# Performance work log

Measured on AMD Instinct MI355X. Metric: run time of the kernel, lower is better.

## Reference

```python
import jax, jax.numpy as jnp
import numpy as np

B, T = 256, 800
D_IN, H, L, V = 128, 512, 2, 128


def setup_inputs() -> dict:
    key = jax.random.key(0)
    ks = jax.random.split(key, 12)
    s = 0.1  # init scale for stability
    return {
        "W_ih0": jax.random.normal(ks[0], (4 * H, D_IN), jnp.float32) * s,
        "W_hh0": jax.random.normal(ks[1], (4 * H, H), jnp.float32) * s,
        "b_ih0": jax.random.normal(ks[2], (4 * H,), jnp.float32) * s,
        "b_hh0": jax.random.normal(ks[3], (4 * H,), jnp.float32) * s,
        "W_ih1": jax.random.normal(ks[4], (4 * H, H), jnp.float32) * s,
        "W_hh1": jax.random.normal(ks[5], (4 * H, H), jnp.float32) * s,
        "b_ih1": jax.random.normal(ks[6], (4 * H,), jnp.float32) * s,
        "b_hh1": jax.random.normal(ks[7], (4 * H,), jnp.float32) * s,
        "W_lin": jax.random.normal(ks[8], (V, H), jnp.float32) * s,
        "b_lin": jax.random.normal(ks[9], (V,), jnp.float32) * s,
        "z": jax.random.randint(ks[10], (B, T), 0, V, jnp.int32),
        "num_frames": jax.random.randint(ks[11], (B,), 100, 800, jnp.int32),
    }


def _lstm_log_prob(layers, W_lin, b_lin, z, num_frames):
    # teacher-forced inputs: step i sees one_hot(z[:, i-1]), zeros at i=0
    oh = jax.nn.one_hot(z[:, :-1], D_IN, dtype=jnp.float32)          # [B, T-1, D]
    inputs = jnp.concatenate([jnp.zeros((B, 1, D_IN), jnp.float32), oh], axis=1)
    inputs = jnp.transpose(inputs, (1, 0, 2))                         # [T, B, D]

    def step(carry, x_t):
        h, c = carry  # each [L, B, H]
        inp = x_t
        hs, cs = [], []
        for l, (Wih, Whh, bih, bhh) in enumerate(layers):
            gates = inp @ Wih.T + h[l] @ Whh.T + bih + bhh            # [B, 4H]
            i, f, g, o = jnp.split(gates, 4, axis=-1)                 # torch gate order i,f,g,o
            c_new = jax.nn.sigmoid(f) * c[l] + jax.nn.sigmoid(i) * jnp.tanh(g)
            h_new = jax.nn.sigmoid(o) * jnp.tanh(c_new)
            hs.append(h_new)
            cs.append(c_new)
            inp = h_new
        logits_t = inp @ W_lin.T + b_lin                              # [B, V]
        return (jnp.stack(hs), jnp.stack(cs)), logits_t

    h0 = jnp.zeros((L, B, H), jnp.float32)
    c0 = jnp.zeros((L, B, H), jnp.float32)
    _, logits = jax.lax.scan(step, (h0, c0), inputs)                  # [T, B, V]
    logits = jnp.transpose(logits, (1, 0, 2))                         # [B, T, V]

    logp = jax.nn.log_softmax(logits, axis=-1)
    nll = -jnp.take_along_axis(logp, z[..., None].astype(jnp.int32), axis=-1)[..., 0]  # [B, T]
    mask = (jnp.arange(T)[None, :] < num_frames[:, None]).astype(nll.dtype)
    return (nll * mask).mean(axis=-1)                                 # [B] (mean over full T, as in torch)


def reference(W_ih0, W_hh0, b_ih0, b_hh0, W_ih1, W_hh1, b_ih1, b_hh1, W_lin, b_lin, z, num_frames):
    layers = [(W_ih0, W_hh0, b_ih0, b_hh0), (W_ih1, W_hh1, b_ih1, b_hh1)]
    return _lstm_log_prob(layers, W_lin, b_lin, z, num_frames)
```

## Files before the change

kernel.cpp:

```cpp
#include <hip/hip_runtime.h>

#define TT 800

typedef __attribute__((ext_vector_type(8))) short bf16x8;
typedef __attribute__((ext_vector_type(4))) float f32x4;
typedef unsigned short u16;
typedef unsigned int u32;
typedef unsigned long long u64;

constexpr int NCW = 128, NWG = 136, RT = 32;
constexpr size_t WL0A_OFF = 0;
constexpr size_t WL0B_OFF = 2097152;
constexpr size_t WL1_OFF  = 2621440;
constexpr size_t WLIN_OFF = 6815744;
constexpr size_t H0_OFF   = 6946816;
constexpr size_t H1_OFF   = 7471104;
constexpr size_t BAR_OFF  = 7995392;
constexpr int HB = 256 * 512;
constexpr int A_ST = 520;
constexpr int G_OFF_B = 33280;
constexpr int P_OFF_B = 49792;
constexpr int LDS_BYTES = 53248;

__device__ __forceinline__ u16 f2b(float x) {
  u32 u = __float_as_uint(x);
  return (u16)((u + 0x7FFFu + ((u >> 16) & 1u)) >> 16);
}
__device__ __forceinline__ float b2f(u16 v) { return __uint_as_float(((u32)v) << 16); }
__device__ __forceinline__ float sigf(float x) { return 1.f / (1.f + __expf(-x)); }
__device__ __forceinline__ float tanh_f(float x) { float e = __expf(2.f * x); return 1.f - 2.f / (e + 1.f); }

__device__ __forceinline__ u64 ld_coh8(const u64* p) {
  return __hip_atomic_load(p, __ATOMIC_RELAXED, __HIP_MEMORY_SCOPE_AGENT);
}
__device__ __forceinline__ void st_coh8(u64* p, u64 v) {
  __hip_atomic_store(p, v, __ATOMIC_RELAXED, __HIP_MEMORY_SCOPE_AGENT);
}
__device__ __forceinline__ void fadd(u32* f) {
  __hip_atomic_fetch_add(f, 1u, __ATOMIC_RELAXED, __HIP_MEMORY_SCOPE_AGENT);
}
__device__ __forceinline__ void fpoll(u32* f, u32 thr) {
  while (__hip_atomic_load(f, __ATOMIC_RELAXED, __HIP_MEMORY_SCOPE_AGENT) < thr)
    __builtin_amdgcn_s_sleep(1);
}
__device__ __forceinline__ void fadd_l(u32* f) {
  __hip_atomic_fetch_add(f, 1u, __ATOMIC_RELAXED, __HIP_MEMORY_SCOPE_WORKGROUP);
}
__device__ __forceinline__ void fpoll_l(u32* f, u32 thr) {
  while (*(volatile u32*)f < thr) {
    __builtin_amdgcn_s_sleep(1);
    asm volatile("buffer_inv" ::: "memory");
  }
}
__device__ __forceinline__ void l1inv() { asm volatile("buffer_inv" ::: "memory"); }

__global__ void prep_kernel(const float* __restrict__ wih0, const float* __restrict__ whh0,
                            const float* __restrict__ wih1, const float* __restrict__ whh1,
                            const float* __restrict__ wlinf,
                            u16* __restrict__ wl0a, u16* __restrict__ wl0b,
                            u16* __restrict__ wl1, u16* __restrict__ wlin) {
  int i = blockIdx.x * 256 + threadIdx.x;
  const int NA = 2048 * 512, NB = 128 * 2048, N1 = 2048 * 1024, N2 = 128 * 512;
  if (i < NA) {
    int col = i >> 9, k = i & 511;
    wl0a[i] = f2b(whh0[col * 512 + k]);
  } else if (i < NA + NB) {
    int j = i - NA, k = j >> 11, col = j & 2047;
    wl0b[j] = f2b(wih0[col * 128 + k]);
  } else if (i < NA + NB + N1) {
    int j = i - NA - NB, col = j >> 10, k = j & 1023;
    float v = (k < 512) ? wih1[col * 512 + k] : whh1[col * 512 + (k - 512)];
    wl1[j] = f2b(v);
  } else if (i < NA + NB + N1 + N2) {
    int j = i - NA - NB - N1, col = j >> 9, k = j & 511;
    wlin[j] = f2b(wlinf[col * 512 + k]);
  }
}

__global__ __launch_bounds__(256, 1) void lstm_kernel(
    const float* __restrict__ bih0, const float* __restrict__ bhh0,
    const float* __restrict__ bih1, const float* __restrict__ bhh1,
    const float* __restrict__ blin,
    const int* __restrict__ z, const int* __restrict__ nfr,
    const u16* __restrict__ wl0a, const u16* __restrict__ wl0b,
    const u16* __restrict__ wl1, const u16* __restrict__ wlin,
    u16* __restrict__ h0buf, u16* __restrict__ h1buf,
    u32* __restrict__ bars, float* __restrict__ out) {
  extern __shared__ char smem[];
  u16* A = (u16*)smem;
  float* Gf = (float*)(smem + G_OFF_B);
  float* Pm = (float*)(smem + P_OFF_B);
  float* Ps = Pm + 256;
  float* Pt = Ps + 256;
  const int wg = blockIdx.x;
  const int w_all = wg >> 3;
  const bool isC = (w_all < 16);
  const int tile = wg & 7;
  const int w = isC ? w_all : 16;
  const int tid = threadIdx.x, lane = tid & 63, wv = tid >> 6;
  const int l15 = lane & 15, l4 = lane >> 4;
  const int row0 = tile * RT;
  u32* F = bars + tile * 32;
  const f32x4 VZ = {0.f, 0.f, 0.f, 0.f};
  const int rC = tid >> 3, u0C = (tid & 7) * 4;
  const int cuL = tid & 31, rgL = tid >> 5;

  float c0s[4] = {0, 0, 0, 0}, c1s[4] = {0, 0, 0, 0};
  float accN = 0.f, nflv = 0.f;
  float bias0c[2], bias1c[2], biasLc[2];
  bf16x8 bq0R[32];
  bf16x8 bq1R[64];
  bf16x8 wlR[32];

  if (isC) {
#pragma unroll
    for (int cb = 0; cb < 2; ++cb) {
      int col = wv * 512 + w * 32 + cb * 16 + l15;
      bias0c[cb] = bih0[col] + bhh0[col];
      bias1c[cb] = bih1[col] + bhh1[col];
      const u16* b0 = wl0a + (size_t)col * 512 + l4 * 8;
#pragma unroll
      for (int kb = 0; kb < 16; ++kb) bq0R[cb * 16 + kb] = *(const bf16x8*)(b0 + kb * 32);
      const u16* b1 = wl1 + (size_t)col * 1024 + l4 * 8;
#pragma unroll
      for (int kb = 0; kb < 32; ++kb) bq1R[cb * 32 + kb] = *(const bf16x8*)(b1 + kb * 32);
    }
  } else {
#pragma unroll
    for (int cb = 0; cb < 2; ++cb) {
      int colV = wv * 32 + cb * 16 + l15;
      biasLc[cb] = blin[colV];
      const u16* bL = wlin + (size_t)colV * 512 + l4 * 8;
#pragma unroll
      for (int kb = 0; kb < 16; ++kb) wlR[cb * 16 + kb] = *(const bf16x8*)(bL + kb * 32);
    }
    if (rgL == 0) nflv = (float)nfr[row0 + cuL];
  }

  u32 xcc;
  asm volatile("s_getreg_b32 %0, hwreg(HW_REG_XCC_ID)" : "=s"(xcc));
  {
    int* hls = (int*)Pm;
    if (tid == 0) {
      u32 bit = 1u << (xcc & 31u);
      __hip_atomic_fetch_or(bars + 256 + tile, bit, __ATOMIC_RELAXED, __HIP_MEMORY_SCOPE_AGENT);
      __hip_atomic_fetch_add(bars + 272, 1u, __ATOMIC_RELAXED, __HIP_MEMORY_SCOPE_AGENT);
      while (__hip_atomic_load(bars + 272, __ATOMIC_RELAXED, __HIP_MEMORY_SCOPE_AGENT) < (u32)NWG)
        __builtin_amdgcn_s_sleep(1);
      u32 m = __hip_atomic_load(bars + 256 + tile, __ATOMIC_RELAXED, __HIP_MEMORY_SCOPE_AGENT);
      hls[0] = (m == bit) ? 1 : 0;
    }
    __syncthreads();
    const_cast<volatile int&>(hls[0]);
  }
  const bool lok = (((volatile int*)Pm)[0] != 0);
  __syncthreads();

  if (isC && w == 0) {
    u64* z0 = (u64*)(h0buf + HB + row0 * 512);
    u64* z1 = (u64*)(h1buf + row0 * 512);
    u64* z2 = (u64*)(h1buf + HB + row0 * 512);
    if (lok) {
      for (int k = tid; k < 2048; k += 256) { z0[k] = 0; z1[k] = 0; z2[k] = 0; }
    } else {
      for (int k = tid; k < 2048; k += 256) { st_coh8(z0 + k, 0); st_coh8(z1 + k, 0); st_coh8(z2 + k, 0); }
    }
  }
  __syncthreads();
  if (tid == 0) { if (lok) fadd_l(F); else fadd(F); }

  auto ldA = [&](int rb, int kb) {
    return *(const bf16x8*)(A + (rb * 16 + l15) * A_ST + kb * 32 + l4 * 8);
  };

#pragma unroll 1
  for (int tau = 0; tau <= TT + 1; ++tau) {
    if (tid == 0) { if (lok) fpoll_l(F, 17u * (u32)(tau + 1)); else fpoll(F, 17u * (u32)(tau + 1)); }
    __syncthreads();
    if (lok) l1inv();
    const u16* h0src = h0buf + ((tau + 1) & 1) * HB + row0 * 512;
    const u64* h1s64 = (const u64*)(h1buf + (tau & 1) * HB + row0 * 512);
    const bool l0act = isC && (tau < TT);
    const bool l1act = isC && (tau >= 1 && tau <= TT);

    if (isC) {
      if (tau <= TT) {
        u64 ta[8], tb[8];
        const u64* s64 = (const u64*)h0src;
        if (lok) {
#pragma unroll
          for (int c = 0; c < 8; ++c) {
            int li = c * 256 + tid;
            ta[c] = s64[li * 2]; tb[c] = s64[li * 2 + 1];
          }
        } else {
#pragma unroll
          for (int c = 0; c < 8; ++c) {
            int li = c * 256 + tid;
            ta[c] = ld_coh8(s64 + li * 2); tb[c] = ld_coh8(s64 + li * 2 + 1);
          }
        }
#pragma unroll
        for (int c = 0; c < 8; ++c) {
          int li = c * 256 + tid, row = li >> 6, cc = li & 63;
          u64* d = (u64*)(A + row * A_ST + cc * 8);
          d[0] = ta[c]; d[1] = tb[c];
        }
      }
      u64 ha[4], hb[4];
      if (l1act) {
        if (lok) {
#pragma unroll
          for (int c = 0; c < 4; ++c) {
            int li = c * 256 + tid;
            ha[c] = h1s64[li * 2]; hb[c] = h1s64[li * 2 + 1];
          }
        } else {
#pragma unroll
          for (int c = 0; c < 4; ++c) {
            int li = c * 256 + tid;
            ha[c] = ld_coh8(h1s64 + li * 2); hb[c] = ld_coh8(h1s64 + li * 2 + 1);
          }
        }
      }
      __syncthreads();

      f32x4 acc0[2][2] = {{VZ, VZ}, {VZ, VZ}};
      f32x4 acc1[2][2] = {{VZ, VZ}, {VZ, VZ}};
      if (l0act) {
#pragma unroll
        for (int kb = 0; kb < 16; ++kb) {
          bf16x8 a0 = ldA(0, kb), a1 = ldA(1, kb);
#pragma unroll
          for (int cb = 0; cb < 2; ++cb) {
            acc0[0][cb] = __builtin_amdgcn_mfma_f32_16x16x32_bf16(a0, bq0R[cb * 16 + kb], acc0[0][cb], 0, 0, 0);
            acc0[1][cb] = __builtin_amdgcn_mfma_f32_16x16x32_bf16(a1, bq0R[cb * 16 + kb], acc0[1][cb], 0, 0, 0);
          }
        }
      }
      if (l1act) {
#pragma unroll
        for (int kb = 0; kb < 16; ++kb) {
          bf16x8 a0 = ldA(0, kb), a1 = ldA(1, kb);
#pragma unroll
          for (int cb = 0; cb < 2; ++cb) {
            acc1[0][cb] = __builtin_amdgcn_mfma_f32_16x16x32_bf16(a0, bq1R[cb * 32 + kb], acc1[0][cb], 0, 0, 0);
            acc1[1][cb] = __builtin_amdgcn_mfma_f32_16x16x32_bf16(a1, bq1R[cb * 32 + kb], acc1[1][cb], 0, 0, 0);
          }
        }
      }
      if (l0act) {
#pragma unroll
        for (int rb = 0; rb < 2; ++rb)
#pragma unroll
          for (int cb = 0; cb < 2; ++cb)
#pragma unroll
            for (int q = 0; q < 4; ++q)
              Gf[(rb * 16 + l4 * 4 + q) * 129 + wv * 32 + cb * 16 + l15] = acc0[rb][cb][q] + bias0c[cb];
      }
      __syncthreads();

      u64 ha2[4], hb2[4];
      if (l1act) {
        if (lok) {
#pragma unroll
          for (int c = 0; c < 4; ++c) {
            int li = (c + 4) * 256 + tid;
            ha2[c] = h1s64[li * 2]; hb2[c] = h1s64[li * 2 + 1];
          }
        } else {
#pragma unroll
          for (int c = 0; c < 4; ++c) {
            int li = (c + 4) * 256 + tid;
            ha2[c] = ld_coh8(h1s64 + li * 2); hb2[c] = ld_coh8(h1s64 + li * 2 + 1);
          }
        }
      }
      if (l0act) {
        float g4[4][4];
#pragma unroll
        for (int g = 0; g < 4; ++g)
#pragma unroll
          for (int j = 0; j < 4; ++j) g4[g][j] = Gf[rC * 129 + g * 32 + u0C + j];
        if (tau >= 1) {
          int zr = z[(row0 + rC) * TT + (tau - 1)];
          const u16* gb = wl0b + (size_t)zr * 2048 + w * 32 + u0C;
#pragma unroll
          for (int g = 0; g < 4; ++g) {
            u64 v = *(const u64*)(gb + g * 512);
#pragma unroll
            for (int j = 0; j < 4; ++j) g4[g][j] += b2f((u16)(v >> (16 * j)));
          }
        }
        u64 pk = 0;
#pragma unroll
        for (int j = 0; j < 4; ++j) {
          float cn = sigf(g4[1][j]) * c0s[j] + sigf(g4[0][j]) * tanh_f(g4[2][j]);
          float hn = sigf(g4[3][j]) * tanh_f(cn);
          c0s[j] = cn;
          pk |= ((u64)f2b(hn)) << (16 * j);
        }
        u16* h0w = h0buf + (tau & 1) * HB + row0 * 512;
        u64* dst = (u64*)(h0w + rC * 512 + w * 32 + u0C);
        if (lok) *dst = pk; else st_coh8(dst, pk);
      }
      if (l1act) {
#pragma unroll
        for (int c = 0; c < 4; ++c) {
          int li = c * 256 + tid, row = li >> 6, cc = li & 63;
          u64* d = (u64*)(A + row * A_ST + cc * 8);
          d[0] = ha[c]; d[1] = hb[c];
        }
#pragma unroll
        for (int c = 0; c < 4; ++c) {
          int li = (c + 4) * 256 + tid, row = li >> 6, cc = li & 63;
          u64* d = (u64*)(A + row * A_ST + cc * 8);
          d[0] = ha2[c]; d[1] = hb2[c];
        }
      }
      __syncthreads();

      if (l1act) {
#pragma unroll
        for (int kb = 16; kb < 32; ++kb) {
          bf16x8 a0 = ldA(0, kb - 16), a1 = ldA(1, kb - 16);
#pragma unroll
          for (int cb = 0; cb < 2; ++cb) {
            acc1[0][cb] = __builtin_amdgcn_mfma_f32_16x16x32_bf16(a0, bq1R[cb * 32 + kb], acc1[0][cb], 0, 0, 0);
            acc1[1][cb] = __builtin_amdgcn_mfma_f32_16x16x32_bf16(a1, bq1R[cb * 32 + kb], acc1[1][cb], 0, 0, 0);
          }
        }
#pragma unroll
        for (int rb = 0; rb < 2; ++rb)
#pragma unroll
          for (int cb = 0; cb < 2; ++cb)
#pragma unroll
            for (int q = 0; q < 4; ++q)
              Gf[(rb * 16 + l4 * 4 + q) * 129 + wv * 32 + cb * 16 + l15] = acc1[rb][cb][q] + bias1c[cb];
      }
      __syncthreads();

      if (l1act) {
        float g4[4][4];
#pragma unroll
        for (int g = 0; g < 4; ++g)
#pragma unroll
          for (int j = 0; j < 4; ++j) g4[g][j] = Gf[rC * 129 + g * 32 + u0C + j];
        u64 pk = 0;
#pragma unroll
        for (int j = 0; j < 4; ++j) {
          float cn = sigf(g4[1][j]) * c1s[j] + sigf(g4[0][j]) * tanh_f(g4[2][j]);
          float hn = sigf(g4[3][j]) * tanh_f(cn);
          c1s[j] = cn;
          pk |= ((u64)f2b(hn)) << (16 * j);
        }
        u16* h1w = h1buf + ((tau + 1) & 1) * HB + row0 * 512;
        u64* dst = (u64*)(h1w + rC * 512 + w * 32 + u0C);
        if (lok) *dst = pk; else st_coh8(dst, pk);
      }
      __syncthreads();
      if (tid == 0) { if (lok) fadd_l(F); else fadd(F); }
    } else {
      const bool lgact = (tau >= 2);
      if (lgact) {
        u64 ta[8], tb[8];
        if (lok) {
#pragma unroll
          for (int c = 0; c < 8; ++c) {
            int li = c * 256 + tid;
            ta[c] = h1s64[li * 2]; tb[c] = h1s64[li * 2 + 1];
          }
        } else {
#pragma unroll
          for (int c = 0; c < 8; ++c) {
            int li = c * 256 + tid;
            ta[c] = ld_coh8(h1s64 + li * 2); tb[c] = ld_coh8(h1s64 + li * 2 + 1);
          }
        }
#pragma unroll
        for (int c = 0; c < 8; ++c) {
          int li = c * 256 + tid, row = li >> 6, cc = li & 63;
          u64* d = (u64*)(A + row * A_ST + cc * 8);
          d[0] = ta[c]; d[1] = tb[c];
        }
      }
      __syncthreads();
      if (tid == 0) { if (lok) fadd_l(F); else fadd(F); }
      if (lgact) {
        f32x4 accL[2][2] = {{VZ, VZ}, {VZ, VZ}};
#pragma unroll
        for (int kb = 0; kb < 16; ++kb) {
          bf16x8 a0 = ldA(0, kb), a1 = ldA(1, kb);
#pragma unroll
          for (int cb = 0; cb < 2; ++cb) {
            accL[0][cb] = __builtin_amdgcn_mfma_f32_16x16x32_bf16(a0, wlR[cb * 16 + kb], accL[0][cb], 0, 0, 0);
            accL[1][cb] = __builtin_amdgcn_mfma_f32_16x16x32_bf16(a1, wlR[cb * 16 + kb], accL[1][cb], 0, 0, 0);
          }
        }
#pragma unroll
        for (int rb = 0; rb < 2; ++rb)
#pragma unroll
          for (int cb = 0; cb < 2; ++cb)
#pragma unroll
            for (int q = 0; q < 4; ++q)
              Gf[(rb * 16 + l4 * 4 + q) * 129 + wv * 32 + cb * 16 + l15] = accL[rb][cb][q] + biasLc[cb];
      }
      __syncthreads();
      if (lgact) {
        int t2 = tau - 2;
        int r = cuL, k = rgL;
        float vloc[16], mloc = -3.4e38f;
#pragma unroll
        for (int j = 0; j < 16; ++j) {
          vloc[j] = Gf[r * 129 + k * 16 + j];
          mloc = fmaxf(mloc, vloc[j]);
        }
        Pm[r * 8 + k] = mloc;
        __syncthreads();
        float mrow = Pm[r * 8];
#pragma unroll
        for (int j = 1; j < 8; ++j) mrow = fmaxf(mrow, Pm[r * 8 + j]);
        int zr = z[(row0 + r) * TT + t2];
        float sloc = 0.f, tloc = 0.f;
#pragma unroll
        for (int j = 0; j < 16; ++j) {
          sloc += __expf(vloc[j] - mrow);
          tloc += (k * 16 + j == zr) ? vloc[j] : 0.f;
        }
        Ps[r * 8 + k] = sloc; Pt[r * 8 + k] = tloc;
        __syncthreads();
        if (k == 0) {
          float s = 0.f, tv = 0.f;
#pragma unroll
          for (int j = 0; j < 8; ++j) { s += Ps[r * 8 + j]; tv += Pt[r * 8 + j]; }
          if ((float)t2 < nflv) accN += mrow + __logf(s) - tv;
        }
      } else {
        __syncthreads(); __syncthreads();
      }
    }
  }

  if (!isC && rgL == 0) out[row0 + cuL] = accN * (1.0f / TT);
}

extern "C" void kernel_launch(void* const* d_in, const int* in_sizes, int n_in,
                              void* d_out, int out_size, void* d_ws, size_t ws_size,
                              hipStream_t stream) {
  const float* wih0 = (const float*)d_in[0];
  const float* whh0 = (const float*)d_in[1];
  const float* bih0 = (const float*)d_in[2];
  const float* bhh0 = (const float*)d_in[3];
  const float* wih1 = (const float*)d_in[4];
  const float* whh1 = (const float*)d_in[5];
  const float* bih1 = (const float*)d_in[6];
  const float* bhh1 = (const float*)d_in[7];
  const float* wlinf = (const float*)d_in[8];
  const float* blin = (const float*)d_in[9];
  const int* z = (const int*)d_in[10];
  const int* nfr = (const int*)d_in[11];
  float* out = (float*)d_out;
  char* ws = (char*)d_ws;
  u16* wl0a = (u16*)(ws + WL0A_OFF);
  u16* wl0b = (u16*)(ws + WL0B_OFF);
  u16* wl1 = (u16*)(ws + WL1_OFF);
  u16* wlin = (u16*)(ws + WLIN_OFF);
  u16* h0buf = (u16*)(ws + H0_OFF);
  u16* h1buf = (u16*)(ws + H1_OFF);
  u32* bars = (u32*)(ws + BAR_OFF);

  hipMemsetAsync(ws + BAR_OFF, 0, 2048, stream);
  const int NTOT = 2048 * 512 + 128 * 2048 + 2048 * 1024 + 128 * 512;
  prep_kernel<<<dim3((NTOT + 255) / 256), dim3(256), 0, stream>>>(
      wih0, whh0, wih1, whh1, wlinf, wl0a, wl0b, wl1, wlin);
  lstm_kernel<<<dim3(NWG), dim3(256), LDS_BYTES, stream>>>(
      bih0, bhh0, bih1, bhh1, blin, z, nfr, wl0a, wl0b, wl1, wlin, h0buf, h1buf, bars, out);
}
```

Measured before the change: 7.665 ms.

## Split per-tile step barrier into separate layer-0 and layer-1 flags

Replaces the single per-tile counter barrier with two flags. F0 tracks only layer-0 hidden-state completion among the 16 compute workgroups, and F1 tracks layer-1 plus the output-projection workgroup. Compute workgroups now wait only on F0 before starting the layer-0 matmul, then poll F1 before loading h1. They also signal F0 as soon as layer-0 h is written, so the next step's layer-0 can begin earlier and the two layers overlap across workgroups. The cost is an extra poll and extra __syncthreads per step, and h1 loads are no longer prefetched before the layer-0 matmul.

```diff
diff --git a/kernel.cpp b/kernel.cpp
--- a/kernel.cpp
+++ b/kernel.cpp
@@ -100,7 +100,8 @@
   const int tid = threadIdx.x, lane = tid & 63, wv = tid >> 6;
   const int l15 = lane & 15, l4 = lane >> 4;
   const int row0 = tile * RT;
-  u32* F = bars + tile * 32;
+  u32* F0 = bars + tile * 32;
+  u32* F1 = bars + tile * 32 + 16;
   const f32x4 VZ = {0.f, 0.f, 0.f, 0.f};
   const int rC = tid >> 3, u0C = (tid & 7) * 4;
   const int cuL = tid & 31, rgL = tid >> 5;
@@ -167,7 +168,13 @@
     }
   }
   __syncthreads();
-  if (tid == 0) { if (lok) fadd_l(F); else fadd(F); }
+  if (tid == 0) {
+    if (isC) {
+      if (lok) { fadd_l(F0); fadd_l(F1); } else { fadd(F0); fadd(F1); }
+    } else {
+      if (lok) fadd_l(F1); else fadd(F1);
+    }
+  }
 
   auto ldA = [&](int rb, int kb) {
     return *(const bf16x8*)(A + (rb * 16 + l15) * A_ST + kb * 32 + l4 * 8);
@@ -175,15 +182,15 @@
 
 #pragma unroll 1
   for (int tau = 0; tau <= TT + 1; ++tau) {
-    if (tid == 0) { if (lok) fpoll_l(F, 17u * (u32)(tau + 1)); else fpoll(F, 17u * (u32)(tau + 1)); }
-    __syncthreads();
-    if (lok) l1inv();
     const u16* h0src = h0buf + ((tau + 1) & 1) * HB + row0 * 512;
     const u64* h1s64 = (const u64*)(h1buf + (tau & 1) * HB + row0 * 512);
     const bool l0act = isC && (tau < TT);
     const bool l1act = isC && (tau >= 1 && tau <= TT);
 
     if (isC) {
+      if (tid == 0) { if (lok) fpoll_l(F0, 16u * (u32)(tau + 1)); else fpoll(F0, 16u * (u32)(tau + 1)); }
+      __syncthreads();
+      if (lok) l1inv();
       if (tau <= TT) {
         u64 ta[8], tb[8];
         const u64* s64 = (const u64*)h0src;
@@ -207,22 +214,6 @@
           d[0] = ta[c]; d[1] = tb[c];
         }
       }
-      u64 ha[4], hb[4];
-      if (l1act) {
-        if (lok) {
-#pragma unroll
-          for (int c = 0; c < 4; ++c) {
-            int li = c * 256 + tid;
-            ha[c] = h1s64[li * 2]; hb[c] = h1s64[li * 2 + 1];
-          }
-        } else {
-#pragma unroll
-          for (int c = 0; c < 4; ++c) {
-            int li = c * 256 + tid;
-            ha[c] = ld_coh8(h1s64 + li * 2); hb[c] = ld_coh8(h1s64 + li * 2 + 1);
-          }
-        }
-      }
       __syncthreads();
 
       f32x4 acc0[2][2] = {{VZ, VZ}, {VZ, VZ}};
@@ -260,19 +251,22 @@
       }
       __syncthreads();
 
-      u64 ha2[4], hb2[4];
+      if (tid == 0) { if (lok) fpoll_l(F1, 17u * (u32)(tau + 1)); else fpoll(F1, 17u * (u32)(tau + 1)); }
+      __syncthreads();
+
+      u64 ha[8], hb[8];
       if (l1act) {
         if (lok) {
 #pragma unroll
-          for (int c = 0; c < 4; ++c) {
-            int li = (c + 4) * 256 + tid;
-            ha2[c] = h1s64[li * 2]; hb2[c] = h1s64[li * 2 + 1];
+          for (int c = 0; c < 8; ++c) {
+            int li = c * 256 + tid;
+            ha[c] = h1s64[li * 2]; hb[c] = h1s64[li * 2 + 1];
           }
         } else {
 #pragma unroll
-          for (int c = 0; c < 4; ++c) {
-            int li = (c + 4) * 256 + tid;
-            ha2[c] = ld_coh8(h1s64 + li * 2); hb2[c] = ld_coh8(h1s64 + li * 2 + 1);
+          for (int c = 0; c < 8; ++c) {
+            int li = c * 256 + tid;
+            ha[c] = ld_coh8(h1s64 + li * 2); hb[c] = ld_coh8(h1s64 + li * 2 + 1);
           }
         }
       }
@@ -304,18 +298,15 @@
         u64* dst = (u64*)(h0w + rC * 512 + w * 32 + u0C);
         if (lok) *dst = pk; else st_coh8(dst, pk);
       }
+      __syncthreads();
+      if (tid == 0) { if (lok) fadd_l(F0); else fadd(F0); }
+
       if (l1act) {
 #pragma unroll
-        for (int c = 0; c < 4; ++c) {
+        for (int c = 0; c < 8; ++c) {
           int li = c * 256 + tid, row = li >> 6, cc = li & 63;
           u64* d = (u64*)(A + row * A_ST + cc * 8);
           d[0] = ha[c]; d[1] = hb[c];
-        }
-#pragma unroll
-        for (int c = 0; c < 4; ++c) {
-          int li = (c + 4) * 256 + tid, row = li >> 6, cc = li & 63;
-          u64* d = (u64*)(A + row * A_ST + cc * 8);
-          d[0] = ha2[c]; d[1] = hb2[c];
         }
       }
       __syncthreads();
@@ -359,9 +350,12 @@
         if (lok) *dst = pk; else st_coh8(dst, pk);
       }
       __syncthreads();
-      if (tid == 0) { if (lok) fadd_l(F); else fadd(F); }
+      if (tid == 0) { if (lok) fadd_l(F1); else fadd(F1); }
     } else {
       const bool lgact = (tau >= 2);
+      if (tid == 0) { if (lok) fpoll_l(F1, 17u * (u32)(tau + 1)); else fpoll(F1, 17u * (u32)(tau + 1)); }
+      __syncthreads();
+      if (lok) l1inv();
       if (lgact) {
         u64 ta[8], tb[8];
         if (lok) {
@@ -385,7 +379,7 @@
         }
       }
       __syncthreads();
-      if (tid == 0) { if (lok) fadd_l(F); else fadd(F); }
+      if (tid == 0) { if (lok) fadd_l(F1); else fadd(F1); }
       if (lgact) {
         f32x4 accL[2][2] = {{VZ, VZ}, {VZ, VZ}};
 #pragma unroll
```

Result: slower. 8.147 ms (+6.3%).
